# Kernel optimization log

Measured on AMD Instinct MI355X. Metric: run time of the kernel, lower is better.

The kernel has to match this reference:

```python
import jax, jax.numpy as jnp
import numpy as np

N = 4_000_000   # samples
V = 16          # num_variables
L = 4           # num_layers -> 8 leaves, internal levels of sizes 4, 2, 1


def setup_inputs() -> dict:
    key = jax.random.key(0)
    ks = jax.random.split(key, 12)
    inp = {
        "x": jax.random.uniform(ks[0], (N, V), jnp.float32, 1.0, 10.0),
        "leaf_w": jax.random.normal(ks[1], (8, V), jnp.float32),
        "leaf_b": jax.random.normal(ks[2], (8,), jnp.float32),
        "w1": jax.random.normal(ks[3], (1,), jnp.float32),
        "b1": jax.random.normal(ks[4], (1,), jnp.float32),
        "om1": jax.random.normal(ks[5], (1, 4), jnp.float32),
        "w2": jax.random.normal(ks[6], (2,), jnp.float32),
        "b2": jax.random.normal(ks[7], (2,), jnp.float32),
        "om2": jax.random.normal(ks[8], (2, 4), jnp.float32),
        "w3": jax.random.normal(ks[9], (4,), jnp.float32),
        "b3": jax.random.normal(ks[10], (4,), jnp.float32),
        "om3": jax.random.normal(ks[11], (4, 4), jnp.float32),
    }
    return inp


def _level_up(h, w, b, om):
    # h: [2n, N] hidden values of children; combine sibling pairs.
    l, r = h[0::2], h[1::2]           # each [n, N]
    s = l + r
    # operations = ['+', 'sin', 'cos', '*'] per operator_p
    ops = jnp.stack([s, jnp.sin(s), jnp.cos(s), l * r])   # [4, n, N]
    omega = jax.nn.softmax(om, axis=-1)                   # [n, 4] (standard-softmax phase)
    comb = jnp.einsum('no,onb->nb', omega, ops)           # [n, N]
    return w[:, None] * comb + b[:, None]


def reference(x, leaf_w, leaf_b, w1, b1, om1, w2, b2, om2, w3, b3, om3):
    # leaves: h_j = leaf_w[j] @ x^T + leaf_b[j]  -> [8, N]
    h = jnp.einsum('lv,nv->ln', leaf_w, x) + leaf_b[:, None]
    h = _level_up(h, w3, b3, om3)   # level closest to leaves: 4 nodes
    h = _level_up(h, w2, b2, om2)   # 2 nodes
    h = _level_up(h, w1, b1, om1)   # root: 1 node
    return h[0]                     # [N]
```

## Files before the change

### kernel.cpp

```cpp
#include <hip/hip_runtime.h>


__device__ __forceinline__ float rfl(float v) {
    return __int_as_float(__builtin_amdgcn_readfirstlane(__float_as_int(v)));
}

__device__ __forceinline__ void fast_sincos(float s, float* sn, float* cs) {
#if __has_builtin(__builtin_amdgcn_sinf) && __has_builtin(__builtin_amdgcn_cosf)
    const float INV2PI = 0.15915494309189535f;
    float t = s * INV2PI;
    t = t - floorf(t);
    *sn = __builtin_amdgcn_sinf(t);
    *cs = __builtin_amdgcn_cosf(t);
#else
    sincosf(s, sn, cs);
#endif
}

__device__ __forceinline__ float node_eval(float l, float r, const float c[5]) {
    float s = l + r;
    float sn, cs;
    fast_sincos(s, &sn, &cs);
    float acc = c[4];
    acc = fmaf(c[3], l * r, acc);
    acc = fmaf(c[2], cs, acc);
    acc = fmaf(c[1], sn, acc);
    acc = fmaf(c[0], s,  acc);
    return acc;
}

__global__ __launch_bounds__(256) void tree_fused(const float4* __restrict__ x,
                                                  const float* __restrict__ lw,
                                                  const float* __restrict__ lb,
                                                  const float* __restrict__ w1, const float* __restrict__ b1,
                                                  const float* __restrict__ om1,
                                                  const float* __restrict__ w2, const float* __restrict__ b2,
                                                  const float* __restrict__ om2,
                                                  const float* __restrict__ w3, const float* __restrict__ b3,
                                                  const float* __restrict__ om3,
                                                  float* __restrict__ out, int N) {
    float cf[7][5];
#pragma unroll
    for (int nd = 0; nd < 7; ++nd) {
        const float* om;
        float w, b;
        if (nd < 4)      { om = om3 + nd * 4;       w = w3[nd];     b = b3[nd]; }
        else if (nd < 6) { om = om2 + (nd - 4) * 4; w = w2[nd - 4]; b = b2[nd - 4]; }
        else             { om = om1;                w = w1[0];      b = b1[0]; }
        float m  = fmaxf(fmaxf(om[0], om[1]), fmaxf(om[2], om[3]));
        float e0 = __expf(om[0] - m), e1 = __expf(om[1] - m);
        float e2 = __expf(om[2] - m), e3 = __expf(om[3] - m);
        float inv = w / (e0 + e1 + e2 + e3);
        cf[nd][0] = rfl(e0 * inv); cf[nd][1] = rfl(e1 * inv);
        cf[nd][2] = rfl(e2 * inv); cf[nd][3] = rfl(e3 * inv);
        cf[nd][4] = rfl(b);
    }

    int stride = gridDim.x * 256;
    for (int n = blockIdx.x * 256 + threadIdx.x; n < N; n += stride) {
        const float4* xp = x + (size_t)n * 4;
        float4 a0 = xp[0], a1 = xp[1], a2 = xp[2], a3 = xp[3];
        float xv[16] = {a0.x, a0.y, a0.z, a0.w, a1.x, a1.y, a1.z, a1.w,
                        a2.x, a2.y, a2.z, a2.w, a3.x, a3.y, a3.z, a3.w};

        float h[8];
#pragma unroll
        for (int l = 0; l < 8; ++l) {
            float acc = lb[l];
#pragma unroll
            for (int v = 0; v < 16; ++v) acc = fmaf(lw[l * 16 + v], xv[v], acc);
            h[l] = acc;
        }

        float g4[4];
#pragma unroll
        for (int nd = 0; nd < 4; ++nd) g4[nd] = node_eval(h[2 * nd], h[2 * nd + 1], cf[nd]);
        float g2[2];
        g2[0] = node_eval(g4[0], g4[1], cf[4]);
        g2[1] = node_eval(g4[2], g4[3], cf[5]);
        out[n] = node_eval(g2[0], g2[1], cf[6]);
    }
}

extern "C" void kernel_launch(void* const* d_in, const int* in_sizes, int n_in,
                              void* d_out, int out_size, void* d_ws, size_t ws_size,
                              hipStream_t stream) {
    const float* x      = (const float*)d_in[0];
    const float* leaf_w = (const float*)d_in[1];
    const float* leaf_b = (const float*)d_in[2];
    const float* w1     = (const float*)d_in[3];
    const float* b1     = (const float*)d_in[4];
    const float* om1    = (const float*)d_in[5];
    const float* w2     = (const float*)d_in[6];
    const float* b2     = (const float*)d_in[7];
    const float* om2    = (const float*)d_in[8];
    const float* w3     = (const float*)d_in[9];
    const float* b3     = (const float*)d_in[10];
    const float* om3    = (const float*)d_in[11];

    int N = in_sizes[0] / 16;
    float* out = (float*)d_out;

    int blocks = 2048;
    tree_fused<<<blocks, 256, 0, stream>>>((const float4*)x, leaf_w, leaf_b,
                                           w1, b1, om1, w2, b2, om2, w3, b3, om3,
                                           out, N);
}
```

Before: 50.94 us.

## Stage input rows through per-wave LDS for coalesced global loads

Each wave now loads a 64-row tile of x with fully coalesced 16-byte loads (consecutive lanes read consecutive float4s), writes it into a padded LDS buffer (row stride 17 to avoid bank conflicts), then each lane reads its own 16-float row back from LDS. This replaces the per-thread strided 64-byte row loads, which spread each wave's accesses across many cache lines per instruction. It adds LDS traffic and relies on a manual lgkmcnt wait without a barrier, which is only valid because each wave uses its own private buffer. It also assumes N is divisible by 64, since the tail is dropped.

```diff
diff --git a/kernel.cpp b/kernel.cpp
--- a/kernel.cpp
+++ b/kernel.cpp
@@ -1,5 +1,7 @@
 #include <hip/hip_runtime.h>
 
+
+typedef float f32x4 __attribute__((ext_vector_type(4)));
 
 __device__ __forceinline__ float rfl(float v) {
     return __int_as_float(__builtin_amdgcn_readfirstlane(__float_as_int(v)));
@@ -29,7 +31,9 @@
     return acc;
 }
 
-__global__ __launch_bounds__(256) void tree_fused(const float4* __restrict__ x,
+#define ROW_F 17
+
+__global__ __launch_bounds__(256) void tree_fused(const f32x4* __restrict__ x,
                                                   const float* __restrict__ lw,
                                                   const float* __restrict__ lb,
                                                   const float* __restrict__ w1, const float* __restrict__ b1,
@@ -38,7 +42,12 @@
                                                   const float* __restrict__ om2,
                                                   const float* __restrict__ w3, const float* __restrict__ b3,
                                                   const float* __restrict__ om3,
-                                                  float* __restrict__ out, int N) {
+                                                  float* __restrict__ out, int nTiles) {
+    __shared__ float lds[4][64 * ROW_F];
+    const int wave = threadIdx.x >> 6;
+    const int lane = threadIdx.x & 63;
+    float* myLds = lds[wave];
+
     float cf[7][5];
 #pragma unroll
     for (int nd = 0; nd < 7; ++nd) {
@@ -56,12 +65,23 @@
         cf[nd][4] = rfl(b);
     }
 
-    int stride = gridDim.x * 256;
-    for (int n = blockIdx.x * 256 + threadIdx.x; n < N; n += stride) {
-        const float4* xp = x + (size_t)n * 4;
-        float4 a0 = xp[0], a1 = xp[1], a2 = xp[2], a3 = xp[3];
-        float xv[16] = {a0.x, a0.y, a0.z, a0.w, a1.x, a1.y, a1.z, a1.w,
-                        a2.x, a2.y, a2.z, a2.w, a3.x, a3.y, a3.z, a3.w};
+    const int gwave  = blockIdx.x * 4 + wave;
+    const int nWaves = gridDim.x * 4;
+
+    for (int tile = gwave; tile < nTiles; tile += nWaves) {
+        const f32x4* src = x + (size_t)tile * 256;
+#pragma unroll
+        for (int i = 0; i < 4; ++i) {
+            int j = i * 64 + lane;
+            f32x4 v = src[j];
+            float* p = myLds + (j >> 2) * ROW_F + (j & 3) * 4;
+            p[0] = v.x; p[1] = v.y; p[2] = v.z; p[3] = v.w;
+        }
+        asm volatile("s_waitcnt lgkmcnt(0)" ::: "memory");
+
+        float xv[16];
+#pragma unroll
+        for (int v = 0; v < 16; ++v) xv[v] = myLds[lane * ROW_F + v];
 
         float h[8];
 #pragma unroll
@@ -78,7 +98,7 @@
         float g2[2];
         g2[0] = node_eval(g4[0], g4[1], cf[4]);
         g2[1] = node_eval(g4[2], g4[3], cf[5]);
-        out[n] = node_eval(g2[0], g2[1], cf[6]);
+        out[tile * 64 + lane] = node_eval(g2[0], g2[1], cf[6]);
     }
 }
 
@@ -99,10 +119,11 @@
     const float* om3    = (const float*)d_in[11];
 
     int N = in_sizes[0] / 16;
+    int nTiles = N / 64;
     float* out = (float*)d_out;
 
     int blocks = 2048;
-    tree_fused<<<blocks, 256, 0, stream>>>((const float4*)x, leaf_w, leaf_b,
+    tree_fused<<<blocks, 256, 0, stream>>>((const f32x4*)x, leaf_w, leaf_b,
                                            w1, b1, om1, w2, b2, om2, w3, b3, om3,
-                                           out, N);
+                                           out, nTiles);
 }
```

Result: slower. 53.73 us (+5.5%).
